# Optimization experiments

Measured on AMD Instinct MI355X. Metric: run time of the kernel, lower is better.

Reference implementation:

```python
import jax, jax.numpy as jnp
import numpy as np

N, F_IN, F_OUT = 2048, 128, 64


def setup_inputs() -> dict:
    key = jax.random.key(0)
    k0, k1, k2, k3, k4 = jax.random.split(key, 5)
    node_features = jax.random.normal(k0, (N, F_IN), dtype=jnp.float32)
    adjacency_matrix = jax.random.uniform(k1, (N, N), dtype=jnp.float32)
    mask_father = jax.random.uniform(k2, (N, N), dtype=jnp.float32)
    mask_hadamard = jax.random.uniform(k3, (N, N), dtype=jnp.float32)
    # kaiming_uniform (fan_in, relu): bound = sqrt(6 / fan_in) * sqrt(2) adjustment -> gain*sqrt(3/fan_in)
    bound = np.sqrt(2.0) * np.sqrt(3.0 / F_IN)
    weight = jax.random.uniform(k4, (F_IN, F_OUT), dtype=jnp.float32, minval=-bound, maxval=bound)
    bias = jnp.zeros((F_OUT,), dtype=jnp.float32)
    return {
        "node_features": node_features,
        "adjacency_matrix": adjacency_matrix,
        "mask_father": mask_father,
        "mask_hadamard": mask_hadamard,
        "weight": weight,
        "bias": bias,
    }


def reference(node_features, adjacency_matrix, mask_father, mask_hadamard, weight, bias):
    # H[i,f] = (X @ W + b)[i,f]
    H = node_features @ weight + bias  # [N, F]
    # Original math: out[j,f] = sum_k mf[j,k] * H[k,f] * (sum_i A[j,i] * H[i,f] * mh[i,k])
    # G[j,f,k] corresponds to the (masked hadamard @ adjacency) intermediate [N, F, N]
    G = jnp.einsum('ji,if,ik->jfk', adjacency_matrix, H, mask_hadamard)
    out = jnp.einsum('jfk,kf,jk->jf', G, H, mask_father)
    return out
```

## Files before the change

kernel.cpp:

```cpp
#include <hip/hip_runtime.h>
#include <hip/hip_bf16.h>


typedef __attribute__((ext_vector_type(8))) _Float16 f16x8;
typedef __attribute__((ext_vector_type(4))) _Float16 f16x4;
typedef __attribute__((ext_vector_type(4))) float f32x4;

#define N 2048
#define FOUT 64
#define FIN 128
#define NIT 512

#define MFMA16(A,B,C) __builtin_amdgcn_mfma_f32_16x16x32_f16((A),(B),(C),0,0,0)

__device__ __forceinline__ void gl_lds16(const _Float16* g, _Float16* l) {
    __builtin_amdgcn_global_load_lds(
        (const __attribute__((address_space(1))) void*)g,
        (__attribute__((address_space(3))) void*)l, 16, 0, 0);
}


__global__ __launch_bounds__(256) void k_zero(float* __restrict__ out) {
    ((float4*)out)[blockIdx.x * 256 + threadIdx.x] = make_float4(0.f, 0.f, 0.f, 0.f);
}

__global__ __launch_bounds__(256) void k_h(const float* __restrict__ X,
                                           const float* __restrict__ W,
                                           const float* __restrict__ bias,
                                           float* __restrict__ HT,
                                           _Float16* __restrict__ HTh) {
    __shared__ float Ws[FIN * FOUT];
    __shared__ float Xs[4 * FIN];
    int t = threadIdx.x;
#pragma unroll
    for (int s = 0; s < 32; ++s) Ws[t + 256 * s] = W[t + 256 * s];
    int i0 = blockIdx.x * 4;
#pragma unroll
    for (int s = 0; s < 2; ++s) { int idx = t + 256 * s; Xs[idx] = X[(size_t)i0 * FIN + idx]; }
    __syncthreads();
    int f = t & 63, il = t >> 6;
    float h = bias[f];
#pragma unroll
    for (int p = 0; p < FIN; ++p) h = fmaf(Xs[il * FIN + p], Ws[p * FOUT + f], h);
    int i = i0 + il;
    HT[f * N + i] = h;
    HTh[f * N + i] = (_Float16)h;
}

__global__ __launch_bounds__(256) void k_a2h(const float* __restrict__ A,
                                             _Float16* __restrict__ Ah) {
    int g = blockIdx.x * 256 + threadIdx.x;
    float4 v = ((const float4*)A)[g];
    f16x4 o;
    o[0] = (_Float16)v.x; o[1] = (_Float16)v.y; o[2] = (_Float16)v.z; o[3] = (_Float16)v.w;
    ((f16x4*)Ah)[g] = o;
}

__global__ __launch_bounds__(256) void k_mht(const float* __restrict__ mh,
                                             _Float16* __restrict__ mhT) {
    __shared__ float tile[64][65];
    int t = threadIdx.x;
    int bx = blockIdx.x & 31;
    int by = blockIdx.x >> 5;
#pragma unroll
    for (int s = 0; s < 16; ++s) {
        int lin = t + 256 * s;
        int r = lin >> 6, c = lin & 63;
        tile[r][c] = mh[(size_t)(by * 64 + r) * N + bx * 64 + c];
    }
    __syncthreads();
#pragma unroll
    for (int s = 0; s < 16; ++s) {
        int lin = t + 256 * s;
        int kr = lin >> 6, ic = lin & 63;
        mhT[(size_t)(bx * 64 + kr) * N + by * 64 + ic] = (_Float16)tile[ic][kr];
    }
}


#define STAGE(DBUF, IT)                                                        \
  {                                                                            \
    int ib_ = ((IT) & 63) << 5;                                                \
    int kt_ = (IT) >> 6;                                                       \
    const _Float16* pa_ = Ah + a_base + ib_;                                   \
    const _Float16* pb_ = mhT + b_base + (size_t)kt_ * 128 * N + ib_;          \
    _Float16* la_ = &tiles[DBUF][0][w * 1024];                                 \
    _Float16* lb_ = &tiles[DBUF][1][w * 1024];                                 \
    _Pragma("unroll")                                                          \
    for (int c_ = 0; c_ < 2; ++c_) {                                           \
      gl_lds16(pa_ + c_ * 16 * N, la_ + c_ * 512);                             \
      gl_lds16(pb_ + c_ * 16 * N, lb_ + c_ * 512);                             \
    }                                                                          \
  }

#define COMPUTE_HALF(BUF, IT)                                                  \
  {                                                                            \
    const char* hb_ = (const char*)hbuf + (((IT) & 63) << 6);                  \
    f16x8 ar[4], br[4];                                                        \
    _Pragma("unroll")                                                          \
    for (int x_ = 0; x_ < 4; ++x_)                                             \
      ar[x_] = *(const f16x8*)(tbase + (BUF) * 16384 + faA + x_ * 1024);       \
    _Pragma("unroll")                                                          \
    for (int x_ = 0; x_ < 4; ++x_)                                             \
      br[x_] = *(const f16x8*)(tbase + (BUF) * 16384 + 8192 + faB + x_ * 1024);\
    f16x8 h0 = *(const f16x8*)(hb_ + hq);                                      \
    f16x8 h1 = *(const f16x8*)(hb_ + 4096 + hq);                               \
    __builtin_amdgcn_s_setprio(1);                                             \
    _Pragma("unroll")                                                          \
    for (int jj = 0; jj < 4; ++jj) {                                           \
      f16x8 a0 = ar[jj] * h0;                                                  \
      f16x8 a1 = ar[jj] * h1;                                                  \
      _Pragma("unroll")                                                        \
      for (int kk = 0; kk < 4; ++kk) {                                         \
        acc[0][jj][kk] = MFMA16(a0, br[kk], acc[0][jj][kk]);                   \
        acc[1][jj][kk] = MFMA16(a1, br[kk], acc[1][jj][kk]);                   \
      }                                                                        \
    }                                                                          \
    __builtin_amdgcn_s_setprio(0);                                             \
    if (((IT) & 63) == 63) EPILOGUE(IT)                                        \
  }

#define EPILOGUE(IT)                                                           \
  {                                                                            \
    int kb_ = khalf + (((IT) >> 6) << 7);                                      \
    _Pragma("unroll")                                                          \
    for (int jj = 0; jj < 4; ++jj) {                                           \
      float t0[4] = {0.f, 0.f, 0.f, 0.f};                                      \
      float t1[4] = {0.f, 0.f, 0.f, 0.f};                                      \
      int jrow = jbase + wj + jj * 16 + q * 4;                                 \
      _Pragma("unroll")                                                        \
      for (int kk = 0; kk < 4; ++kk) {                                         \
        int kg = kb_ + wk + kk * 16 + l16;                                     \
        float hk0 = HT[f0 * N + kg];                                           \
        float hk1 = HT[(f0 + 1) * N + kg];                                     \
        _Pragma("unroll")                                                      \
        for (int r = 0; r < 4; ++r) {                                          \
          float m = mf[(size_t)(jrow + r) * N + kg];                           \
          t0[r] = fmaf(acc[0][jj][kk][r], m * hk0, t0[r]);                     \
          t1[r] = fmaf(acc[1][jj][kk][r], m * hk1, t1[r]);                     \
        }                                                                      \
      }                                                                        \
      _Pragma("unroll")                                                        \
      for (int r = 0; r < 4; ++r) {                                            \
        float v0 = t0[r], v1 = t1[r];                                          \
        v0 += __shfl_xor(v0, 1); v1 += __shfl_xor(v1, 1);                      \
        v0 += __shfl_xor(v0, 2); v1 += __shfl_xor(v1, 2);                      \
        v0 += __shfl_xor(v0, 4); v1 += __shfl_xor(v1, 4);                      \
        v0 += __shfl_xor(v0, 8); v1 += __shfl_xor(v1, 8);                      \
        if (l16 == 0) {                                                        \
          red[0][w][jj * 16 + q * 4 + r] += v0;                                \
          red[1][w][jj * 16 + q * 4 + r] += v1;                                \
        }                                                                      \
      }                                                                        \
    }                                                                          \
    _Pragma("unroll")                                                          \
    for (int a_ = 0; a_ < 4; ++a_)                                             \
      _Pragma("unroll")                                                        \
      for (int b_ = 0; b_ < 4; ++b_) {                                         \
        acc[0][a_][b_] = (f32x4){0.f, 0.f, 0.f, 0.f};                          \
        acc[1][a_][b_] = (f32x4){0.f, 0.f, 0.f, 0.f};                          \
      }                                                                        \
  }

__global__ __launch_bounds__(256, 2) void k_main(const float* __restrict__ mf,
                                                 const float* __restrict__ HT,
                                                 const _Float16* __restrict__ HTh,
                                                 const _Float16* __restrict__ Ah,
                                                 const _Float16* __restrict__ mhT,
                                                 float* __restrict__ out) {
    __shared__ _Float16 tiles[2][2][128 * 32];
    __shared__ _Float16 hbuf[2][N];
    __shared__ float red[2][4][64];

    int t = threadIdx.x;
    int jbase = (blockIdx.x >> 6) << 7;
    int f0 = ((blockIdx.x >> 1) & 31) << 1;
    int khalf = (blockIdx.x & 1) << 10;
    int w = t >> 6, lane = t & 63, q = lane >> 4, l16 = lane & 15;
    int wj = (w & 1) << 6, wk = (w >> 1) << 6;

#pragma unroll
    for (int s = 0; s < 2; ++s) {
        int idx = t + 256 * s;
        ((f16x8*)hbuf)[idx] = *(const f16x8*)&HTh[(size_t)(f0 + (idx >> 8)) * N + (idx & 255) * 8];
    }
    ((float*)red)[t] = 0.f;
    ((float*)red)[t + 256] = 0.f;

    int chlog = (lane & 3) ^ ((lane >> 3) & 3);
    size_t a_base = (size_t)(jbase + w * 32 + (lane >> 2)) * N + chlog * 8;
    size_t b_base = (size_t)(khalf + w * 32 + (lane >> 2)) * N + chlog * 8;

    const char* tbase = (const char*)&tiles[0][0][0];
    int chr = (q ^ ((l16 >> 1) & 3)) * 16;
    int faA = (wj + l16) * 64 + chr;
    int faB = (wk + l16) * 64 + chr;
    int hq = q * 16;

    STAGE(0, 0)

    f32x4 acc[2][4][4];
#pragma unroll
    for (int a = 0; a < 4; ++a)
#pragma unroll
        for (int b = 0; b < 4; ++b) {
            acc[0][a][b] = (f32x4){0.f, 0.f, 0.f, 0.f};
            acc[1][a][b] = (f32x4){0.f, 0.f, 0.f, 0.f};
        }

    for (int tp = 0; tp < NIT / 2; ++tp) {
        int it0 = tp * 2;
        __syncthreads();
        STAGE(1, it0 + 1)
        COMPUTE_HALF(0, it0)
        __syncthreads();
        if (tp != NIT / 2 - 1) STAGE(0, it0 + 2)
        COMPUTE_HALF(1, it0 + 1)
    }

    __syncthreads();
    if (t < 128) {
        int j = t;
#pragma unroll
        for (int fi = 0; fi < 2; ++fi) {
            float v = (j < 64) ? (red[fi][0][j] + red[fi][2][j])
                               : (red[fi][1][j - 64] + red[fi][3][j - 64]);
            atomicAdd(&out[(size_t)(jbase + j) * FOUT + f0 + fi], v);
        }
    }
}

extern "C" void kernel_launch(void* const* d_in, const int* in_sizes, int n_in,
                              void* d_out, int out_size, void* d_ws, size_t ws_size,
                              hipStream_t stream) {
    const float* X    = (const float*)d_in[0];
    const float* A    = (const float*)d_in[1];
    const float* mf   = (const float*)d_in[2];
    const float* mh   = (const float*)d_in[3];
    const float* W    = (const float*)d_in[4];
    const float* bias = (const float*)d_in[5];
    float* out = (float*)d_out;

    float*    HT  = (float*)d_ws;
    _Float16* HTh = (_Float16*)((char*)d_ws + 524288);
    _Float16* Ah  = (_Float16*)((char*)d_ws + 1048576);
    _Float16* mhT = (_Float16*)((char*)d_ws + 1048576 + 8388608);

    k_zero<<<(N * FOUT / 4) / 256, 256, 0, stream>>>(out);
    k_h<<<N / 4, 256, 0, stream>>>(X, W, bias, HT, HTh);
    k_a2h<<<(N * N / 4) / 256, 256, 0, stream>>>(A, Ah);
    k_mht<<<(N / 64) * (N / 64), 256, 0, stream>>>(mh, mhT);
    k_main<<<16 * 32 * 2, 256, 0, stream>>>(mf, HT, HTh, Ah, mhT, out);
}
```

Baseline: 1.049 ms.

## Give each wave private LDS tiles and replace block barriers with vmcnt waits

```diff
diff --git a/kernel.cpp b/kernel.cpp
--- a/kernel.cpp
+++ b/kernel.cpp
@@ -78,16 +78,20 @@
 }
 
 
+#define WAITV8 { asm volatile("s_waitcnt vmcnt(8)" ::: "memory"); __builtin_amdgcn_sched_barrier(0); }
+#define WAITV0 { asm volatile("s_waitcnt vmcnt(0)" ::: "memory"); __builtin_amdgcn_sched_barrier(0); }
+#define SB0 __builtin_amdgcn_sched_barrier(0);
+
 #define STAGE(DBUF, IT)                                                        \
   {                                                                            \
     int ib_ = ((IT) & 63) << 5;                                                \
     int kt_ = (IT) >> 6;                                                       \
     const _Float16* pa_ = Ah + a_base + ib_;                                   \
     const _Float16* pb_ = mhT + b_base + (size_t)kt_ * 128 * N + ib_;          \
-    _Float16* la_ = &tiles[DBUF][0][w * 1024];                                 \
-    _Float16* lb_ = &tiles[DBUF][1][w * 1024];                                 \
-    _Pragma("unroll")                                                          \
-    for (int c_ = 0; c_ < 2; ++c_) {                                           \
+    _Float16* la_ = &tiles[w][DBUF][0][0];                                     \
+    _Float16* lb_ = &tiles[w][DBUF][1][0];                                     \
+    _Pragma("unroll")                                                          \
+    for (int c_ = 0; c_ < 4; ++c_) {                                           \
       gl_lds16(pa_ + c_ * 16 * N, la_ + c_ * 512);                             \
       gl_lds16(pb_ + c_ * 16 * N, lb_ + c_ * 512);                             \
     }                                                                          \
@@ -99,10 +103,10 @@
     f16x8 ar[4], br[4];                                                        \
     _Pragma("unroll")                                                          \
     for (int x_ = 0; x_ < 4; ++x_)                                             \
-      ar[x_] = *(const f16x8*)(tbase + (BUF) * 16384 + faA + x_ * 1024);       \
+      ar[x_] = *(const f16x8*)(tbase + frbA + (BUF) * 8192 + x_ * 1024);       \
     _Pragma("unroll")                                                          \
     for (int x_ = 0; x_ < 4; ++x_)                                             \
-      br[x_] = *(const f16x8*)(tbase + (BUF) * 16384 + 8192 + faB + x_ * 1024);\
+      br[x_] = *(const f16x8*)(tbase + frbB + (BUF) * 8192 + x_ * 1024);       \
     f16x8 h0 = *(const f16x8*)(hb_ + hq);                                      \
     f16x8 h1 = *(const f16x8*)(hb_ + 4096 + hq);                               \
     __builtin_amdgcn_s_setprio(1);                                             \
@@ -168,7 +172,7 @@
                                                  const _Float16* __restrict__ Ah,
                                                  const _Float16* __restrict__ mhT,
                                                  float* __restrict__ out) {
-    __shared__ _Float16 tiles[2][2][128 * 32];
+    __shared__ _Float16 tiles[4][2][2][2048];
     __shared__ _Float16 hbuf[2][N];
     __shared__ float red[2][4][64];
 
@@ -188,16 +192,17 @@
     ((float*)red)[t + 256] = 0.f;
 
     int chlog = (lane & 3) ^ ((lane >> 3) & 3);
-    size_t a_base = (size_t)(jbase + w * 32 + (lane >> 2)) * N + chlog * 8;
-    size_t b_base = (size_t)(khalf + w * 32 + (lane >> 2)) * N + chlog * 8;
-
-    const char* tbase = (const char*)&tiles[0][0][0];
+    size_t a_base = (size_t)(jbase + wj + (lane >> 2)) * N + chlog * 8;
+    size_t b_base = (size_t)(khalf + wk + (lane >> 2)) * N + chlog * 8;
+
+    const char* tbase = (const char*)&tiles[0][0][0][0];
     int chr = (q ^ ((l16 >> 1) & 3)) * 16;
-    int faA = (wj + l16) * 64 + chr;
-    int faB = (wk + l16) * 64 + chr;
+    int frbA = w * 16384 + l16 * 64 + chr;
+    int frbB = frbA + 4096;
     int hq = q * 16;
 
     STAGE(0, 0)
+    __syncthreads();
 
     f32x4 acc[2][4][4];
 #pragma unroll
@@ -210,11 +215,17 @@
 
     for (int tp = 0; tp < NIT / 2; ++tp) {
         int it0 = tp * 2;
-        __syncthreads();
+        SB0
         STAGE(1, it0 + 1)
+        WAITV8
         COMPUTE_HALF(0, it0)
-        __syncthreads();
-        if (tp != NIT / 2 - 1) STAGE(0, it0 + 2)
+        SB0
+        if (tp != NIT / 2 - 1) {
+            STAGE(0, it0 + 2)
+            WAITV8
+        } else {
+            WAITV0
+        }
         COMPUTE_HALF(1, it0 + 1)
     }
 
```

New measurement: 1.222 ms. +16.5%, slower.
